# Performance work log

Measured on AMD Instinct MI355X. Metric: run time of the kernel, lower is better.

## Reference

```python
import jax, jax.numpy as jnp
import numpy as np

COMMITMENT = 0.25
THRESHOLD = 0.6
SNR_DB = 30.0  # eval_snr_db default-ish channel condition (fixed for determinism)
LN_EPS = 1e-5


def _layernorm(x, g, b):
    m = jnp.mean(x, axis=-1, keepdims=True)
    v = jnp.var(x, axis=-1, keepdims=True)
    return (x - m) * jax.lax.rsqrt(v + LN_EPS) * g + b


def _vq(x, codebook):
    # x: [T, D], codebook: [K, D]. Nearest-neighbor quantize + per-token VQ loss + STE.
    d = (x * x).sum(-1, keepdims=True) - 2.0 * (x @ codebook.T) + (codebook * codebook).sum(-1)  # [T, K]
    idx = jnp.argmin(d, axis=-1)
    q = codebook[idx]  # [T, D]
    loss = (COMMITMENT * jnp.mean((x - jax.lax.stop_gradient(q)) ** 2, axis=-1)
            + jnp.mean((jax.lax.stop_gradient(x) - q) ** 2, axis=-1))  # [T]
    q_ste = x + jax.lax.stop_gradient(q - x)
    return q_ste, loss


def setup_inputs() -> dict:
    key = jax.random.key(0)
    ks = jax.random.split(key, 8)
    B, N, De, Dq, Dd = 64, 196, 768, 512, 256
    return {
        'x_tokens': jax.random.normal(ks[0], (B, N, De), jnp.float32),
        'fim_logits': jax.random.normal(ks[1], (B, N, 1), jnp.float32),
        'W_proj': jax.random.normal(ks[2], (De, Dq), jnp.float32) * (1.0 / np.sqrt(De)),
        'b_proj': jnp.zeros((Dq,), jnp.float32),
        'ln_g': jnp.ones((Dq,), jnp.float32),
        'ln_b': jnp.zeros((Dq,), jnp.float32),
        'cb_high': jax.random.normal(ks[3], (4096, Dq), jnp.float32),
        'cb_low': jax.random.normal(ks[4], (256, Dq), jnp.float32),
        'W_dec': jax.random.normal(ks[5], (Dq, Dd), jnp.float32) * (1.0 / np.sqrt(Dq)),
        'b_dec': jnp.zeros((Dd,), jnp.float32),
        'h_ri': jax.random.normal(ks[6], (B, 2), jnp.float32),
        'noise': jax.random.normal(ks[7], (B, N, Dq), jnp.float32),
    }


def reference(x_tokens, fim_logits, W_proj, b_proj, ln_g, ln_b, cb_high, cb_low, W_dec, b_dec, h_ri, noise):
    B, N, _ = x_tokens.shape
    score = jax.nn.sigmoid(fim_logits[..., 0])          # [B, N]
    route_high = score > THRESHOLD                       # [B, N] bool

    x_proj = _layernorm(x_tokens @ W_proj + b_proj, ln_g, ln_b)  # [B, N, Dq]
    D = x_proj.shape[-1]
    xf = x_proj.reshape(-1, D)
    mf = route_high.reshape(-1)
    sf = score.reshape(-1)

    # Compute both experts densely, select with mask (same math as the masked
    # gather/scatter dispatch in the torch code, jit-friendly static shapes).
    q_high, loss_high = _vq(xf, cb_high)
    q_low, loss_low = _vq(xf, cb_low)
    final = jnp.where(mf[:, None], q_high, q_low).reshape(B, N, D)

    n_high = jnp.maximum(mf.sum(), 1)
    n_low = jnp.maximum((~mf).sum(), 1)
    vq_loss = (jnp.sum(jnp.where(mf, loss_high * sf, 0.0)) / n_high
               + jnp.sum(jnp.where(mf, 0.0, loss_low * (1.0 - sf))) / n_low) / 2.0

    # Rayleigh channel: per-sample fading magnitude h = |CN(0,1)|/sqrt(2), AWGN, equalize.
    n_var = 10.0 ** (-SNR_DB / 10.0)
    h = jnp.sqrt((h_ri ** 2).sum(-1)) / jnp.sqrt(2.0)    # [B]
    h = h[:, None, None]
    y = (h * final + jnp.sqrt(n_var) * noise) / h

    x_dec = y @ W_dec + b_dec                            # [B, N, 256]
    return x_dec, vq_loss
```

## Files before the change

### kernel.cpp

```cpp
#include <hip/hip_runtime.h>
#include <math.h>

#define T_TOK 12544
#define DE 768
#define DQ 512
#define DD 256
#define SEQ 196
#define NCH 4096
#define NCL 256
#define SPL_H 16
#define CODES_PER_BLK 256
#define MARGIN 2.0f
#define CAND_CAP 16

typedef __attribute__((ext_vector_type(8))) short s16x8;
typedef __attribute__((ext_vector_type(4))) float f32x4;

__device__ __forceinline__ float wave_reduce_sum(float v) {
    #pragma unroll
    for (int off = 32; off > 0; off >>= 1) v += __shfl_xor(v, off);
    return v;
}

__device__ __forceinline__ unsigned short f2bf(float f) {
    unsigned int u = __float_as_uint(f);
    u = (u + 0x7fffu + ((u >> 16) & 1u)) >> 16;
    return (unsigned short)u;
}
__device__ __forceinline__ float bf2f(unsigned short h) {
    return __uint_as_float(((unsigned int)h) << 16);
}

__device__ __forceinline__ void gload_lds16(const unsigned short* g, unsigned short* l) {
    __builtin_amdgcn_global_load_lds(
        (const __attribute__((address_space(1))) void*)g,
        (__attribute__((address_space(3))) void*)l,
        16, 0, 0);
}

__device__ __forceinline__ void sumsq_body(const float* __restrict__ cb,
                                           float* __restrict__ cs2,
                                           unsigned short* __restrict__ cbB,
                                           int blk, int NC) {
    int row = blk * 4 + (threadIdx.x >> 6);
    int lane = threadIdx.x & 63;
    if (row >= NC) return;
    const float4* p = (const float4*)(cb + (size_t)row * DQ);
    float4 a = p[lane];
    float4 b = p[lane + 64];
    if (cbB) {
        unsigned short* dst = cbB + (size_t)row * DQ;
        ushort4 ha, hb;
        ha.x = f2bf(a.x); ha.y = f2bf(a.y); ha.z = f2bf(a.z); ha.w = f2bf(a.w);
        hb.x = f2bf(b.x); hb.y = f2bf(b.y); hb.z = f2bf(b.z); hb.w = f2bf(b.w);
        *(ushort4*)(dst + lane * 4) = ha;
        *(ushort4*)(dst + 256 + lane * 4) = hb;
    }
    float s = a.x*a.x + a.y*a.y + a.z*a.z + a.w*a.w
            + b.x*b.x + b.y*b.y + b.z*b.z + b.w*b.w;
    s = wave_reduce_sum(s);
    if (lane == 0) cs2[row] = s;
}

__device__ __forceinline__ void split_body(const float* __restrict__ W, int K, int N,
                                           unsigned short* __restrict__ Thi,
                                           unsigned short* __restrict__ Tlo,
                                           int blk, int nb) {
    int total = K * N;
    for (int idx = blk * 256 + threadIdx.x; idx < total; idx += nb * 256) {
        int n = idx / K, k = idx - n * K;
        float v = W[(size_t)k * N + n];
        unsigned short h = f2bf(v);
        Thi[idx] = h;
        Tlo[idx] = f2bf(v - bf2f(h));
    }
}

__global__ __launch_bounds__(256) void prep_all(const float* __restrict__ cb_h,
                                                float* __restrict__ cs2h,
                                                unsigned short* __restrict__ cbhB,
                                                const float* __restrict__ cb_l,
                                                float* __restrict__ cs2l,
                                                unsigned short* __restrict__ cblB,
                                                const float* __restrict__ Wp,
                                                unsigned short* __restrict__ WThi,
                                                unsigned short* __restrict__ WTlo,
                                                const float* __restrict__ Wd,
                                                unsigned short* __restrict__ WdThi,
                                                unsigned short* __restrict__ WdTlo) {
    int blk = blockIdx.x;
    if (blk < 1024)       sumsq_body(cb_h, cs2h, cbhB, blk, NCH);
    else if (blk < 1088)  sumsq_body(cb_l, cs2l, cblB, blk - 1024, NCL);
    else if (blk < 1600)  split_body(Wp, DE, DQ, WThi, WTlo, blk - 1088, 512);
    else                  split_body(Wd, DQ, DD, WdThi, WdTlo, blk - 1600, 256);
}

template<int NC>
__global__ __launch_bounds__(256) void code_sumsq(const float* __restrict__ cb,
                                                  float* __restrict__ cs2) {
    sumsq_body(cb, cs2, nullptr, blockIdx.x, NC);
}

template<int KDIM, int NSTRIDE, int BN>
__global__ __launch_bounds__(256) void gemm_mfma3(const float* __restrict__ A,
                                                  const unsigned short* __restrict__ BThi,
                                                  const unsigned short* __restrict__ BTlo,
                                                  const float* __restrict__ bias,
                                                  float* __restrict__ out) {
    constexpr int CPW = BN / 64;
    __shared__ __align__(16) unsigned short Ahi[2][64 * 32];
    __shared__ __align__(16) unsigned short Alo[2][64 * 32];
    __shared__ __align__(16) unsigned short Bhi[2][BN * 32];
    __shared__ __align__(16) unsigned short Blo[2][BN * 32];
    const int m0 = blockIdx.x * 64, n0 = blockIdx.y * BN;
    const int tid = threadIdx.x, lane = tid & 63, w = tid >> 6;
    const int stok = tid >> 2, sslot = tid & 3;

    f32x4 acc[4][CPW] = {};
    float4 av0, av1;
    uint4 bh4[CPW], bl4[CPW];

    auto loadStep = [&](int k0) {
        const float* src = A + (size_t)(m0 + stok) * KDIM + k0 + sslot * 8;
        av0 = *(const float4*)src;
        av1 = *(const float4*)(src + 4);
        #pragma unroll
        for (int c = 0; c < CPW; c++) {
            size_t soff = (size_t)(n0 + c * 64 + stok) * KDIM + k0 + sslot * 8;
            bh4[c] = *(const uint4*)(BThi + soff);
            bl4[c] = *(const uint4*)(BTlo + soff);
        }
    };
    auto writeStep = [&](int buf) {
        float xv[8] = {av0.x, av0.y, av0.z, av0.w, av1.x, av1.y, av1.z, av1.w};
        unsigned int hw[4], lw[4];
        #pragma unroll
        for (int j = 0; j < 4; j++) {
            unsigned short h0 = f2bf(xv[2*j]),   h1 = f2bf(xv[2*j+1]);
            unsigned short l0 = f2bf(xv[2*j] - bf2f(h0));
            unsigned short l1 = f2bf(xv[2*j+1] - bf2f(h1));
            hw[j] = (unsigned)h0 | ((unsigned)h1 << 16);
            lw[j] = (unsigned)l0 | ((unsigned)l1 << 16);
        }
        int doffA = stok * 32 + (sslot ^ ((stok >> 1) & 3)) * 8;
        *(uint4*)&Ahi[buf][doffA] = make_uint4(hw[0], hw[1], hw[2], hw[3]);
        *(uint4*)&Alo[buf][doffA] = make_uint4(lw[0], lw[1], lw[2], lw[3]);
        #pragma unroll
        for (int c = 0; c < CPW; c++) {
            int col = c * 64 + stok;
            int doffB = col * 32 + (sslot ^ ((col >> 1) & 3)) * 8;
            *(uint4*)&Bhi[buf][doffB] = bh4[c];
            *(uint4*)&Blo[buf][doffB] = bl4[c];
        }
    };

    loadStep(0); writeStep(0); __syncthreads();
    const int NT = KDIM / 32;
    for (int t = 0; t < NT; t++) {
        const int cur = t & 1;
        if (t + 1 < NT) loadStep((t + 1) * 32);
        const int fr = lane & 15, fs = lane >> 4;
        s16x8 ah[4], al[4];
        #pragma unroll
        for (int tm = 0; tm < 4; tm++) {
            int tok = tm * 16 + fr;
            int off = tok * 32 + (fs ^ ((tok >> 1) & 3)) * 8;
            ah[tm] = *(const s16x8*)&Ahi[cur][off];
            al[tm] = *(const s16x8*)&Alo[cur][off];
        }
        #pragma unroll
        for (int n = 0; n < CPW; n++) {
            int col = w * (16 * CPW) + n * 16 + fr;
            int boff = col * 32 + (fs ^ ((col >> 1) & 3)) * 8;
            s16x8 bh = *(const s16x8*)&Bhi[cur][boff];
            s16x8 bl = *(const s16x8*)&Blo[cur][boff];
            #pragma unroll
            for (int tm = 0; tm < 4; tm++) {
                acc[tm][n] = __builtin_amdgcn_mfma_f32_16x16x32_bf16(ah[tm], bh, acc[tm][n], 0, 0, 0);
                acc[tm][n] = __builtin_amdgcn_mfma_f32_16x16x32_bf16(ah[tm], bl, acc[tm][n], 0, 0, 0);
                acc[tm][n] = __builtin_amdgcn_mfma_f32_16x16x32_bf16(al[tm], bh, acc[tm][n], 0, 0, 0);
            }
        }
        if (t + 1 < NT) writeStep(cur ^ 1);
        __syncthreads();
    }
    const int fr = lane & 15, fg = lane >> 4;
    #pragma unroll
    for (int n = 0; n < CPW; n++) {
        const int col = n0 + w * (16 * CPW) + n * 16 + fr;
        const float bb = bias[col];
        #pragma unroll
        for (int tm = 0; tm < 4; tm++) {
            #pragma unroll
            for (int r = 0; r < 4; r++) {
                int row = m0 + tm * 16 + fg * 4 + r;
                out[(size_t)row * NSTRIDE + col] = acc[tm][n][r] + bb;
            }
        }
    }
}

__global__ __launch_bounds__(256) void proj_gemm(const float* __restrict__ X,
                                                 const float* __restrict__ W,
                                                 const float* __restrict__ bias,
                                                 float* __restrict__ out) {
    __shared__ float As[32][66];
    __shared__ float Bs[32][64];
    const int m0 = blockIdx.x * 64, n0 = blockIdx.y * 64;
    const int tid = threadIdx.x;
    const int tx = tid & 15, ty = tid >> 4;
    float acc[4][4] = {};
    for (int k0 = 0; k0 < DE; k0 += 32) {
        {
            int e = tid;
            int r = e >> 3, c4 = e & 7;
            float4 v = *(const float4*)(X + (size_t)(m0 + r) * DE + k0 + c4 * 4);
            As[c4*4+0][r] = v.x; As[c4*4+1][r] = v.y; As[c4*4+2][r] = v.z; As[c4*4+3][r] = v.w;
            e = tid + 256;
            r = e >> 3; c4 = e & 7;
            v = *(const float4*)(X + (size_t)(m0 + r) * DE + k0 + c4 * 4);
            As[c4*4+0][r] = v.x; As[c4*4+1][r] = v.y; As[c4*4+2][r] = v.z; As[c4*4+3][r] = v.w;
        }
        {
            int e = tid;
            int kk = e >> 4, c4 = e & 15;
            *(float4*)&Bs[kk][c4*4] = *(const float4*)(W + (size_t)(k0 + kk) * DQ + n0 + c4 * 4);
            e = tid + 256;
            kk = e >> 4; c4 = e & 15;
            *(float4*)&Bs[kk][c4*4] = *(const float4*)(W + (size_t)(k0 + kk) * DQ + n0 + c4 * 4);
        }
        __syncthreads();
        #pragma unroll
        for (int k = 0; k < 32; k++) {
            float2 a01 = *(const float2*)&As[k][ty * 4];
            float2 a23 = *(const float2*)&As[k][ty * 4 + 2];
            float4 b = *(const float4*)&Bs[k][tx * 4];
            float av[4] = {a01.x, a01.y, a23.x, a23.y};
            float bv[4] = {b.x, b.y, b.z, b.w};
            #pragma unroll
            for (int i = 0; i < 4; i++)
                #pragma unroll
                for (int j = 0; j < 4; j++)
                    acc[i][j] += av[i] * bv[j];
        }
        __syncthreads();
    }
    float4 bv4 = *(const float4*)(bias + n0 + tx * 4);
    float bb[4] = {bv4.x, bv4.y, bv4.z, bv4.w};
    #pragma unroll
    for (int i = 0; i < 4; i++) {
        int row = m0 + ty * 4 + i;
        float4 o;
        o.x = acc[i][0] + bb[0];
        o.y = acc[i][1] + bb[1];
        o.z = acc[i][2] + bb[2];
        o.w = acc[i][3] + bb[3];
        *(float4*)(out + (size_t)row * DQ + n0 + tx * 4) = o;
    }
}

__global__ __launch_bounds__(256) void ln_route(float* __restrict__ xp,
                                                const float* __restrict__ g,
                                                const float* __restrict__ b,
                                                const float* __restrict__ logits,
                                                float* __restrict__ score,
                                                int* __restrict__ mask,
                                                unsigned short* __restrict__ xpB) {
    int row = blockIdx.x * 4 + (threadIdx.x >> 6);
    int lane = threadIdx.x & 63;
    float* p = xp + (size_t)row * DQ;
    float4 v0 = *(float4*)(p + lane * 4);
    float4 v1 = *(float4*)(p + 256 + lane * 4);
    float s  = v0.x + v0.y + v0.z + v0.w + v1.x + v1.y + v1.z + v1.w;
    float ss = v0.x*v0.x + v0.y*v0.y + v0.z*v0.z + v0.w*v0.w
             + v1.x*v1.x + v1.y*v1.y + v1.z*v1.z + v1.w*v1.w;
    s = wave_reduce_sum(s);
    ss = wave_reduce_sum(ss);
    float m = s * (1.f / DQ);
    float var = ss * (1.f / DQ) - m * m;
    float scale = rsqrtf(var + 1e-5f);
    float4 g0 = *(const float4*)(g + lane * 4);
    float4 g1 = *(const float4*)(g + 256 + lane * 4);
    float4 b0 = *(const float4*)(b + lane * 4);
    float4 b1 = *(const float4*)(b + 256 + lane * 4);
    float4 o0, o1;
    o0.x = (v0.x - m) * scale * g0.x + b0.x;
    o0.y = (v0.y - m) * scale * g0.y + b0.y;
    o0.z = (v0.z - m) * scale * g0.z + b0.z;
    o0.w = (v0.w - m) * scale * g0.w + b0.w;
    o1.x = (v1.x - m) * scale * g1.x + b1.x;
    o1.y = (v1.y - m) * scale * g1.y + b1.y;
    o1.z = (v1.z - m) * scale * g1.z + b1.z;
    o1.w = (v1.w - m) * scale * g1.w + b1.w;
    *(float4*)(p + lane * 4) = o0;
    *(float4*)(p + 256 + lane * 4) = o1;
    if (xpB) {
        unsigned short* dst = xpB + (size_t)row * DQ;
        ushort4 h0, h1;
        h0.x = f2bf(o0.x); h0.y = f2bf(o0.y); h0.z = f2bf(o0.z); h0.w = f2bf(o0.w);
        h1.x = f2bf(o1.x); h1.y = f2bf(o1.y); h1.z = f2bf(o1.z); h1.w = f2bf(o1.w);
        *(ushort4*)(dst + lane * 4) = h0;
        *(ushort4*)(dst + 256 + lane * 4) = h1;
    }
    if (lane == 0) {
        float lg = logits[row];
        float sc = 1.f / (1.f + expf(-lg));
        score[row] = sc;
        mask[row] = sc > 0.6f ? 1 : 0;
    }
}

__global__ __launch_bounds__(1024) void scan_compact(const int* __restrict__ mask,
                                                     int* __restrict__ hlist,
                                                     int* __restrict__ llist,
                                                     int* __restrict__ counts) {
    __shared__ int wsum[16];
    __shared__ int base_h, base_l;
    int tid = threadIdx.x, lane = tid & 63, wid = tid >> 6;
    if (tid == 0) { base_h = 0; base_l = 0; }
    __syncthreads();
    for (int t0 = 0; t0 < T_TOK; t0 += 1024) {
        int t = t0 + tid;
        int valid = t < T_TOK;
        int m = valid ? mask[t] : 0;
        unsigned long long bal = __ballot(m);
        int pre = __popcll(bal & ((1ull << lane) - 1ull));
        if (lane == 0) wsum[wid] = __popcll(bal);
        __syncthreads();
        int woff = 0;
        for (int w = 0; w < wid; w++) woff += wsum[w];
        int btot = 0;
        for (int w = 0; w < 16; w++) btot += wsum[w];
        int vcnt = T_TOK - t0; if (vcnt > 1024) vcnt = 1024;
        int bh = base_h, bl = base_l;
        if (valid) {
            if (m) hlist[bh + woff + pre] = t;
            else   llist[bl + (tid - (woff + pre))] = t;
        }
        __syncthreads();
        if (tid == 0) { base_h = bh + btot; base_l = bl + (vcnt - btot); }
        __syncthreads();
    }
    if (tid == 0) { counts[0] = base_h; counts[1] = base_l; }
}

__global__ __launch_bounds__(256) void vq_mfma_all(const unsigned short* __restrict__ xpB,
                                                   const unsigned short* __restrict__ cbhB,
                                                   const float* __restrict__ cs2h,
                                                   const int* __restrict__ hlist,
                                                   const unsigned short* __restrict__ cblB,
                                                   const float* __restrict__ cs2l,
                                                   const int* __restrict__ llist,
                                                   const int* __restrict__ counts,
                                                   float* __restrict__ smaxH,
                                                   int* __restrict__ scntH,
                                                   uint2* __restrict__ candH,
                                                   float* __restrict__ smaxL,
                                                   int* __restrict__ scntL,
                                                   uint2* __restrict__ candL) {
    const int by = blockIdx.y;
    const unsigned short* cbB; const float* cs2; const int* list;
    float* smax; int* scnt; uint2* cand;
    int count, slice, SPLIT;
    if (by < SPL_H) {
        cbB = cbhB; cs2 = cs2h; list = hlist; count = counts[0];
        slice = by; SPLIT = SPL_H; smax = smaxH; scnt = scntH; cand = candH;
    } else {
        cbB = cblB; cs2 = cs2l; list = llist; count = counts[1];
        slice = 0; SPLIT = 1; smax = smaxL; scnt = scntL; cand = candL;
    }
    const int base = blockIdx.x * 64;
    if (base >= count) return;
    const int cbase = slice * CODES_PER_BLK;

    __shared__ __align__(16) unsigned short Abuf[2 * 64 * 32];
    __shared__ __align__(16) unsigned short Bbuf[2 * 256 * 32];
    __shared__ float wmaxs[4][64];
    __shared__ float tokmax[64];
    __shared__ int ccnt[64];
    __shared__ uint2 cland[64][CAND_CAP];
    __shared__ int rows_s[64];

    const int tid = threadIdx.x;
    const int lane = tid & 63;
    const int w = tid >> 6;
    const int stok = tid >> 2, sslot = tid & 3;

    if (tid < 64) {
        int tl = base + tid;
        rows_s[tid] = list[tl < count ? tl : (count - 1)];
        ccnt[tid] = 0;
    }
    __syncthreads();

    const int swz = sslot ^ ((stok >> 1) & 3);
    const unsigned short* gA  = xpB + (size_t)rows_s[stok] * DQ + swz * 8;
    const unsigned short* gB0 = cbB + (size_t)(cbase + 0 * 64 + stok) * DQ + swz * 8;
    const unsigned short* gB1 = cbB + (size_t)(cbase + 1 * 64 + stok) * DQ + swz * 8;
    const unsigned short* gB2 = cbB + (size_t)(cbase + 2 * 64 + stok) * DQ + swz * 8;
    const unsigned short* gB3 = cbB + (size_t)(cbase + 3 * 64 + stok) * DQ + swz * 8;
    unsigned short* dA = Abuf + w * 512;
    unsigned short* dB = Bbuf + w * 512;

    auto stage = [&](int buf, int k0) {
        gload_lds16(gA  + k0, dA + buf * (64 * 32));
        gload_lds16(gB0 + k0, dB + buf * (256 * 32) + 0 * 2048);
        gload_lds16(gB1 + k0, dB + buf * (256 * 32) + 1 * 2048);
        gload_lds16(gB2 + k0, dB + buf * (256 * 32) + 2 * 2048);
        gload_lds16(gB3 + k0, dB + buf * (256 * 32) + 3 * 2048);
    };

    f32x4 acc[4][4] = {};

    stage(0, 0);
    __syncthreads();
    const int NT = DQ / 32;
    for (int t = 0; t < NT; t++) {
        const int cur = t & 1;
        if (t + 1 < NT) stage(cur ^ 1, (t + 1) * 32);
        const int fr = lane & 15, fs = lane >> 4;
        s16x8 af[4], bf[4];
        #pragma unroll
        for (int tm = 0; tm < 4; tm++) {
            int tok = tm * 16 + fr;
            af[tm] = *(const s16x8*)&Abuf[cur * (64 * 32) + tok * 32 + (fs ^ ((tok >> 1) & 3)) * 8];
        }
        #pragma unroll
        for (int tn = 0; tn < 4; tn++) {
            int cl = w * 64 + tn * 16 + fr;
            bf[tn] = *(const s16x8*)&Bbuf[cur * (256 * 32) + cl * 32 + (fs ^ ((cl >> 1) & 3)) * 8];
        }
        #pragma unroll
        for (int tm = 0; tm < 4; tm++)
            #pragma unroll
            for (int tn = 0; tn < 4; tn++)
                acc[tm][tn] = __builtin_amdgcn_mfma_f32_16x16x32_bf16(af[tm], bf[tn], acc[tm][tn], 0, 0, 0);
        __syncthreads();
    }

    const int fr = lane & 15, fg = lane >> 4;
    float c2[4];
    #pragma unroll
    for (int tn = 0; tn < 4; tn++) c2[tn] = 0.5f * cs2[cbase + w * 64 + tn * 16 + fr];

    #pragma unroll
    for (int tm = 0; tm < 4; tm++) {
        #pragma unroll
        for (int r = 0; r < 4; r++) {
            float m4 = -3.0e38f;
            #pragma unroll
            for (int tn = 0; tn < 4; tn++) {
                float s = acc[tm][tn][r] - c2[tn];
                m4 = fmaxf(m4, s);
            }
            #pragma unroll
            for (int off = 1; off < 16; off <<= 1)
                m4 = fmaxf(m4, __shfl_xor(m4, off));
            if (fr == 0) wmaxs[w][tm * 16 + fg * 4 + r] = m4;
        }
    }
    __syncthreads();
    if (tid < 64)
        tokmax[tid] = fmaxf(fmaxf(wmaxs[0][tid], wmaxs[1][tid]),
                            fmaxf(wmaxs[2][tid], wmaxs[3][tid]));
    __syncthreads();

    #pragma unroll
    for (int tm = 0; tm < 4; tm++) {
        #pragma unroll
        for (int r = 0; r < 4; r++) {
            int token = tm * 16 + fg * 4 + r;
            float thr = tokmax[token] - MARGIN;
            #pragma unroll
            for (int tn = 0; tn < 4; tn++) {
                float s = acc[tm][tn][r] - c2[tn];
                if (s > thr) {
                    int pos = atomicAdd(&ccnt[token], 1);
                    if (pos < CAND_CAP) {
                        uint2 cd;
                        cd.x = __float_as_uint(s);
                        cd.y = (unsigned)(cbase + w * 64 + tn * 16 + fr);
                        cland[token][pos] = cd;
                    }
                }
            }
        }
    }
    __syncthreads();

    if (tid < 64) {
        int tl = base + tid;
        if (tl < count) {
            smax[(size_t)tl * SPLIT + slice] = tokmax[tid];
            scnt[(size_t)tl * SPLIT + slice] = min(ccnt[tid], CAND_CAP);
        }
    }
    for (int i = tid; i < 64 * CAND_CAP; i += 256) {
        int token = i >> 4, j = i & (CAND_CAP - 1);
        int tl = base + token;
        if (tl < count && j < min(ccnt[token], CAND_CAP))
            cand[((size_t)tl * SPLIT + slice) * CAND_CAP + j] = cland[token][j];
    }
}

__global__ __launch_bounds__(256) void vq_rescore_all(float* __restrict__ xp,
                                                      const float* __restrict__ cb_h,
                                                      const float* __restrict__ smaxH,
                                                      const int* __restrict__ scntH,
                                                      const uint2* __restrict__ candH,
                                                      const int* __restrict__ hlist,
                                                      const float* __restrict__ cb_l,
                                                      const float* __restrict__ smaxL,
                                                      const int* __restrict__ scntL,
                                                      const uint2* __restrict__ candL,
                                                      const int* __restrict__ llist,
                                                      const int* __restrict__ counts,
                                                      int* __restrict__ out_idx,
                                                      const float* __restrict__ noise,
                                                      const float* __restrict__ h_ri,
                                                      const float* __restrict__ score,
                                                      float* __restrict__ lh,
                                                      float* __restrict__ ll) {
    const int HB = T_TOK / 4;
    int bx = blockIdx.x;
    const float* cb; const float* smax; const int* scnt; const uint2* cand; const int* list;
    int count, SPLIT, cidx;
    if (bx < HB) {
        cb = cb_h; smax = smaxH; scnt = scntH; cand = candH; list = hlist;
        count = counts[0]; SPLIT = SPL_H; cidx = 0;
    } else {
        bx -= HB;
        cb = cb_l; smax = smaxL; scnt = scntL; cand = candL; list = llist;
        count = counts[1]; SPLIT = 1; cidx = 1;
    }
    const int wid = threadIdx.x >> 6;
    const int lane = threadIdx.x & 63;
    const int tl = bx * 4 + wid;
    if (tl >= count) return;

    float gm = -3.0e38f;
    if (lane < SPLIT) gm = smax[(size_t)tl * SPLIT + lane];
    #pragma unroll
    for (int off = 1; off < 64; off <<= 1)
        gm = fmaxf(gm, __shfl_xor(gm, off));
    const float thr = gm - MARGIN;

    const int t = list[tl];
    float xv[8];
    #pragma unroll
    for (int kk = 0; kk < 8; kk++) xv[kk] = xp[(size_t)t * DQ + lane * 8 + kk];

    double bs = -1.0e300;
    int bi = 0x7fffffff;
    for (int s = 0; s < SPLIT; s++) {
        int cn = scnt[(size_t)tl * SPLIT + s];
        for (int j = 0; j < cn; j++) {
            uint2 cd = cand[((size_t)tl * SPLIT + s) * CAND_CAP + j];
            float av = __uint_as_float(cd.x);
            if (av >= thr) {
                int code = (int)cd.y;
                const float* crow = cb + (size_t)code * DQ;
                double dot = 0.0, nrm = 0.0;
                #pragma unroll
                for (int kk = 0; kk < 8; kk++) {
                    double cv = (double)crow[lane * 8 + kk];
                    dot += (double)xv[kk] * cv;
                    nrm += cv * cv;
                }
                #pragma unroll
                for (int off = 1; off < 64; off <<= 1) {
                    dot += __shfl_xor(dot, off);
                    nrm += __shfl_xor(nrm, off);
                }
                double sc = dot - 0.5 * nrm;
                if (sc > bs || (sc == bs && code < bi)) { bs = sc; bi = code; }
            }
        }
    }
    const float* qrow = cb + (size_t)bi * DQ;
    float4 q0 = *(const float4*)(qrow + lane * 8);
    float4 q1 = *(const float4*)(qrow + lane * 8 + 4);
    const float* nz = noise + (size_t)t * DQ;
    float4 n0 = *(const float4*)(nz + lane * 8);
    float4 n1 = *(const float4*)(nz + lane * 8 + 4);
    float ds = 0.f, dx;
    dx = xv[0] - q0.x; ds += dx * dx;
    dx = xv[1] - q0.y; ds += dx * dx;
    dx = xv[2] - q0.z; ds += dx * dx;
    dx = xv[3] - q0.w; ds += dx * dx;
    dx = xv[4] - q1.x; ds += dx * dx;
    dx = xv[5] - q1.y; ds += dx * dx;
    dx = xv[6] - q1.z; ds += dx * dx;
    dx = xv[7] - q1.w; ds += dx * dx;
    ds = wave_reduce_sum(ds);
    int bbt = t / SEQ;
    float hh0 = h_ri[bbt * 2], hh1 = h_ri[bbt * 2 + 1];
    float hh = sqrtf((hh0 * hh0 + hh1 * hh1) * 0.5f);
    float cc = sqrtf(1e-3f) / hh;
    float4 y0, y1;
    y0.x = q0.x + cc * n0.x; y0.y = q0.y + cc * n0.y;
    y0.z = q0.z + cc * n0.z; y0.w = q0.w + cc * n0.w;
    y1.x = q1.x + cc * n1.x; y1.y = q1.y + cc * n1.y;
    y1.z = q1.z + cc * n1.z; y1.w = q1.w + cc * n1.w;
    *(float4*)(xp + (size_t)t * DQ + lane * 8) = y0;
    *(float4*)(xp + (size_t)t * DQ + lane * 8 + 4) = y1;
    if (lane == 0) {
        out_idx[t] = bi;
        float loss = 1.25f * ds * (1.f / DQ);
        float sc = score[t];
        if (cidx == 0) { lh[t] = loss * sc;  ll[t] = 0.f; }
        else           { lh[t] = 0.f;        ll[t] = loss * (1.f - sc); }
    }
}

template<int NC, int SPLIT>
__global__ __launch_bounds__(256) void vq_partial(const float* __restrict__ xp,
                                                  const float* __restrict__ cb,
                                                  const float* __restrict__ cs2,
                                                  const int* __restrict__ list,
                                                  const int* __restrict__ counts,
                                                  int cidx,
                                                  float* __restrict__ part_s,
                                                  int* __restrict__ part_i) {
    const int count = counts[cidx];
    const int base = blockIdx.x * 64;
    if (base >= count) return;
    const int CODES = NC / SPLIT;
    const int cbase = blockIdx.y * CODES;
    __shared__ float As[32][68];
    __shared__ float Cs[32][68];
    __shared__ int rows_s[64];
    const int tid = threadIdx.x;
    if (tid < 64) {
        int tl = base + tid;
        rows_s[tid] = list[tl < count ? tl : (count - 1)];
    }
    __syncthreads();
    const int tx = tid & 15, ty = tid >> 4;
    float best_s[4];
    int best_i[4];
    #pragma unroll
    for (int i = 0; i < 4; i++) { best_s[i] = -3.0e38f; best_i[i] = 0; }
    for (int c0 = cbase; c0 < cbase + CODES; c0 += 64) {
        float acc[4][4] = {};
        for (int k0 = 0; k0 < DQ; k0 += 32) {
            {
                int e = tid;
                int r = e >> 3, c4 = e & 7;
                float4 v = *(const float4*)(xp + (size_t)rows_s[r] * DQ + k0 + c4 * 4);
                As[c4*4+0][r] = v.x; As[c4*4+1][r] = v.y; As[c4*4+2][r] = v.z; As[c4*4+3][r] = v.w;
                e = tid + 256; r = e >> 3; c4 = e & 7;
                v = *(const float4*)(xp + (size_t)rows_s[r] * DQ + k0 + c4 * 4);
                As[c4*4+0][r] = v.x; As[c4*4+1][r] = v.y; As[c4*4+2][r] = v.z; As[c4*4+3][r] = v.w;
            }
            {
                int e = tid;
                int r = e >> 3, c4 = e & 7;
                float4 v = *(const float4*)(cb + (size_t)(c0 + r) * DQ + k0 + c4 * 4);
                Cs[c4*4+0][r] = v.x; Cs[c4*4+1][r] = v.y; Cs[c4*4+2][r] = v.z; Cs[c4*4+3][r] = v.w;
                e = tid + 256; r = e >> 3; c4 = e & 7;
                v = *(const float4*)(cb + (size_t)(c0 + r) * DQ + k0 + c4 * 4);
                Cs[c4*4+0][r] = v.x; Cs[c4*4+1][r] = v.y; Cs[c4*4+2][r] = v.z; Cs[c4*4+3][r] = v.w;
            }
            __syncthreads();
            #pragma unroll
            for (int k = 0; k < 32; k++) {
                float4 a = *(const float4*)&As[k][ty * 4];
                float4 b = *(const float4*)&Cs[k][tx * 4];
                float av[4] = {a.x, a.y, a.z, a.w};
                float bv[4] = {b.x, b.y, b.z, b.w};
                #pragma unroll
                for (int i = 0; i < 4; i++)
                    #pragma unroll
                    for (int j = 0; j < 4; j++)
                        acc[i][j] += av[i] * bv[j];
            }
            __syncthreads();
        }
        float4 c2v = *(const float4*)(cs2 + c0 + tx * 4);
        float c2[4] = {c2v.x, c2v.y, c2v.z, c2v.w};
        #pragma unroll
        for (int i = 0; i < 4; i++) {
            float s = acc[i][0] - 0.5f * c2[0];
            int bi = c0 + tx * 4;
            #pragma unroll
            for (int j = 1; j < 4; j++) {
                float sj = acc[i][j] - 0.5f * c2[j];
                if (sj > s) { s = sj; bi = c0 + tx * 4 + j; }
            }
            #pragma unroll
            for (int off = 1; off < 16; off <<= 1) {
                float os = __shfl_xor(s, off);
                int oi = __shfl_xor(bi, off);
                if (os > s || (os == s && oi < bi)) { s = os; bi = oi; }
            }
            if (s > best_s[i] || (s == best_s[i] && bi < best_i[i])) {
                best_s[i] = s; best_i[i] = bi;
            }
        }
    }
    if (tx == 0) {
        #pragma unroll
        for (int i = 0; i < 4; i++) {
            int tl = base + ty * 4 + i;
            if (tl < count) {
                part_s[(size_t)tl * SPLIT + blockIdx.y] = best_s[i];
                part_i[(size_t)tl * SPLIT + blockIdx.y] = best_i[i];
            }
        }
    }
}

template<int SPLIT>
__global__ __launch_bounds__(256) void vq_reduce(const float* __restrict__ part_s,
                                                 const int* __restrict__ part_i,
                                                 const int* __restrict__ list,
                                                 const int* __restrict__ counts,
                                                 int cidx,
                                                 int* __restrict__ out_idx) {
    int tl = blockIdx.x * 256 + threadIdx.x;
    if (tl >= counts[cidx]) return;
    float bs = part_s[(size_t)tl * SPLIT];
    int bi = part_i[(size_t)tl * SPLIT];
    #pragma unroll
    for (int s = 1; s < SPLIT; s++) {
        float v = part_s[(size_t)tl * SPLIT + s];
        int vi = part_i[(size_t)tl * SPLIT + s];
        if (v > bs || (v == bs && vi < bi)) { bs = v; bi = vi; }
    }
    out_idx[list[tl]] = bi;
}

__global__ __launch_bounds__(256) void gather_loss_y(float* __restrict__ xp,
                                                     const float* __restrict__ cb_h,
                                                     const float* __restrict__ cb_l,
                                                     const int* __restrict__ idx,
                                                     const float* __restrict__ score,
                                                     const int* __restrict__ mask,
                                                     const float* __restrict__ noise,
                                                     const float* __restrict__ h_ri,
                                                     float* __restrict__ lh,
                                                     float* __restrict__ ll) {
    int t = blockIdx.x * 4 + (threadIdx.x >> 6);
    int lane = threadIdx.x & 63;
    int m = mask[t];
    float sc = score[t];
    const float* q = (m ? cb_h : cb_l) + (size_t)idx[t] * DQ;
    float* x = xp + (size_t)t * DQ;
    const float* nz = noise + (size_t)t * DQ;
    int bb = t / SEQ;
    float h0 = h_ri[bb * 2], h1 = h_ri[bb * 2 + 1];
    float h = sqrtf((h0 * h0 + h1 * h1) * 0.5f);
    float c = sqrtf(1e-3f) / h;
    float4 xv0 = *(float4*)(x + lane * 4);
    float4 xv1 = *(float4*)(x + 256 + lane * 4);
    float4 qv0 = *(const float4*)(q + lane * 4);
    float4 qv1 = *(const float4*)(q + 256 + lane * 4);
    float4 nv0 = *(const float4*)(nz + lane * 4);
    float4 nv1 = *(const float4*)(nz + 256 + lane * 4);
    float dx, ds = 0.f;
    dx = xv0.x - qv0.x; ds += dx * dx;
    dx = xv0.y - qv0.y; ds += dx * dx;
    dx = xv0.z - qv0.z; ds += dx * dx;
    dx = xv0.w - qv0.w; ds += dx * dx;
    dx = xv1.x - qv1.x; ds += dx * dx;
    dx = xv1.y - qv1.y; ds += dx * dx;
    dx = xv1.z - qv1.z; ds += dx * dx;
    dx = xv1.w - qv1.w; ds += dx * dx;
    ds = wave_reduce_sum(ds);
    float4 y0, y1;
    y0.x = qv0.x + c * nv0.x; y0.y = qv0.y + c * nv0.y;
    y0.z = qv0.z + c * nv0.z; y0.w = qv0.w + c * nv0.w;
    y1.x = qv1.x + c * nv1.x; y1.y = qv1.y + c * nv1.y;
    y1.z = qv1.z + c * nv1.z; y1.w = qv1.w + c * nv1.w;
    *(float4*)(x + lane * 4) = y0;
    *(float4*)(x + 256 + lane * 4) = y1;
    if (lane == 0) {
        float loss = 1.25f * ds * (1.f / DQ);
        lh[t] = m ? loss * sc : 0.f;
        ll[t] = m ? 0.f : loss * (1.f - sc);
    }
}

__global__ __launch_bounds__(256) void loss_reduce(const float* __restrict__ lh,
                                                   const float* __restrict__ ll,
                                                   const int* __restrict__ counts,
                                                   float* __restrict__ out) {
    __shared__ float sh[256], sl[256];
    int tid = threadIdx.x;
    float ah = 0.f, al = 0.f;
    for (int t = tid; t < T_TOK; t += 256) { ah += lh[t]; al += ll[t]; }
    sh[tid] = ah; sl[tid] = al;
    __syncthreads();
    for (int o = 128; o > 0; o >>= 1) {
        if (tid < o) { sh[tid] += sh[tid + o]; sl[tid] += sl[tid + o]; }
        __syncthreads();
    }
    if (tid == 0) {
        int nh = counts[0];
        int nl = T_TOK - nh;
        nh = nh > 1 ? nh : 1;
        nl = nl > 1 ? nl : 1;
        out[(size_t)T_TOK * DD] = 0.5f * (sh[0] / (float)nh + sl[0] / (float)nl);
    }
}

__global__ __launch_bounds__(256) void dec_gemm(const float* __restrict__ Y,
                                                const float* __restrict__ W,
                                                const float* __restrict__ bias,
                                                float* __restrict__ out) {
    __shared__ float As[32][66];
    __shared__ float Bs[32][64];
    const int m0 = blockIdx.x * 64, n0 = blockIdx.y * 64;
    const int tid = threadIdx.x;
    const int tx = tid & 15, ty = tid >> 4;
    float acc[4][4] = {};
    for (int k0 = 0; k0 < DQ; k0 += 32) {
        {
            int e = tid;
            int r = e >> 3, c4 = e & 7;
            float4 v = *(const float4*)(Y + (size_t)(m0 + r) * DQ + k0 + c4 * 4);
            As[c4*4+0][r] = v.x; As[c4*4+1][r] = v.y; As[c4*4+2][r] = v.z; As[c4*4+3][r] = v.w;
            e = tid + 256; r = e >> 3; c4 = e & 7;
            v = *(const float4*)(Y + (size_t)(m0 + r) * DQ + k0 + c4 * 4);
            As[c4*4+0][r] = v.x; As[c4*4+1][r] = v.y; As[c4*4+2][r] = v.z; As[c4*4+3][r] = v.w;
        }
        {
            int e = tid;
            int kk = e >> 4, c4 = e & 15;
            *(float4*)&Bs[kk][c4*4] = *(const float4*)(W + (size_t)(k0 + kk) * DD + n0 + c4 * 4);
            e = tid + 256; kk = e >> 4; c4 = e & 15;
            *(float4*)&Bs[kk][c4*4] = *(const float4*)(W + (size_t)(k0 + kk) * DD + n0 + c4 * 4);
        }
        __syncthreads();
        #pragma unroll
        for (int k = 0; k < 32; k++) {
            float2 a01 = *(const float2*)&As[k][ty * 4];
            float2 a23 = *(const float2*)&As[k][ty * 4 + 2];
            float4 b = *(const float4*)&Bs[k][tx * 4];
            float av[4] = {a01.x, a01.y, a23.x, a23.y};
            float bv[4] = {b.x, b.y, b.z, b.w};
            #pragma unroll
            for (int i = 0; i < 4; i++)
                #pragma unroll
                for (int j = 0; j < 4; j++)
                    acc[i][j] += av[i] * bv[j];
        }
        __syncthreads();
    }
    float4 bv4 = *(const float4*)(bias + n0 + tx * 4);
    float bbv[4] = {bv4.x, bv4.y, bv4.z, bv4.w};
    #pragma unroll
    for (int i = 0; i < 4; i++) {
        int row = m0 + ty * 4 + i;
        float4 o;
        o.x = acc[i][0] + bbv[0];
        o.y = acc[i][1] + bbv[1];
        o.z = acc[i][2] + bbv[2];
        o.w = acc[i][3] + bbv[3];
        *(float4*)(out + (size_t)row * DD + n0 + tx * 4) = o;
    }
}

extern "C" void kernel_launch(void* const* d_in, const int* in_sizes, int n_in,
                              void* d_out, int out_size, void* d_ws, size_t ws_size,
                              hipStream_t stream) {
    const float* x_tokens = (const float*)d_in[0];
    const float* fim      = (const float*)d_in[1];
    const float* W_proj   = (const float*)d_in[2];
    const float* b_proj   = (const float*)d_in[3];
    const float* ln_g     = (const float*)d_in[4];
    const float* ln_b     = (const float*)d_in[5];
    const float* cb_high  = (const float*)d_in[6];
    const float* cb_low   = (const float*)d_in[7];
    const float* W_dec    = (const float*)d_in[8];
    const float* b_dec    = (const float*)d_in[9];
    const float* h_ri     = (const float*)d_in[10];
    const float* noise    = (const float*)d_in[11];
    float* out = (float*)d_out;

    char* ws = (char*)d_ws;
    size_t off = 0;
    float* xp = (float*)(ws + off);     off += (size_t)T_TOK * DQ * 4;
    int*   idxb = (int*)(ws + off);     off += (size_t)T_TOK * 4;
    float* score = (float*)(ws + off);  off += (size_t)T_TOK * 4;
    int*   mask = (int*)(ws + off);     off += (size_t)T_TOK * 4;
    float* lh = (float*)(ws + off);     off += (size_t)T_TOK * 4;
    float* ll = (float*)(ws + off);     off += (size_t)T_TOK * 4;
    int*   hlist = (int*)(ws + off);    off += (size_t)T_TOK * 4;
    int*   llist = (int*)(ws + off);    off += (size_t)T_TOK * 4;
    int*   counts = (int*)(ws + off);   off += 64;
    float* cs2h = (float*)(ws + off);   off += (size_t)NCH * 4;
    float* cs2l = (float*)(ws + off);   off += (size_t)NCL * 4;
    size_t off_common = off;

    unsigned short* xpB  = (unsigned short*)(ws + off); off += (size_t)T_TOK * DQ * 2;
    unsigned short* cbhB = (unsigned short*)(ws + off); off += (size_t)NCH * DQ * 2;
    unsigned short* cblB = (unsigned short*)(ws + off); off += (size_t)NCL * DQ * 2;
    float* smaxH = (float*)(ws + off);  off += (size_t)T_TOK * SPL_H * 4;
    int*   scntH = (int*)(ws + off);    off += (size_t)T_TOK * SPL_H * 4;
    uint2* candH = (uint2*)(ws + off);  off += (size_t)T_TOK * SPL_H * CAND_CAP * 8;
    float* smaxL = (float*)(ws + off);  off += (size_t)T_TOK * 4;
    int*   scntL = (int*)(ws + off);    off += (size_t)T_TOK * 4;
    uint2* candL = (uint2*)(ws + off);  off += (size_t)T_TOK * CAND_CAP * 8;
    unsigned short* WThi  = (unsigned short*)(ws + off); off += (size_t)DQ * DE * 2;
    unsigned short* WTlo  = (unsigned short*)(ws + off); off += (size_t)DQ * DE * 2;
    unsigned short* WdThi = (unsigned short*)(ws + off); off += (size_t)DD * DQ * 2;
    unsigned short* WdTlo = (unsigned short*)(ws + off); off += (size_t)DD * DQ * 2;
    size_t need_new = off;
    const bool use_mfma = ws_size >= need_new;

    if (use_mfma) {
        prep_all<<<1856, 256, 0, stream>>>(cb_high, cs2h, cbhB, cb_low, cs2l, cblB,
                                           W_proj, WThi, WTlo, W_dec, WdThi, WdTlo);
        gemm_mfma3<DE, DQ, 64><<<dim3(T_TOK / 64, DQ / 64), 256, 0, stream>>>(
            x_tokens, WThi, WTlo, b_proj, xp);
        ln_route<<<T_TOK / 4, 256, 0, stream>>>(xp, ln_g, ln_b, fim, score, mask, xpB);
        scan_compact<<<1, 1024, 0, stream>>>(mask, hlist, llist, counts);
        vq_mfma_all<<<dim3(T_TOK / 64, SPL_H + 1), 256, 0, stream>>>(
            xpB, cbhB, cs2h, hlist, cblB, cs2l, llist, counts,
            smaxH, scntH, candH, smaxL, scntL, candL);
        vq_rescore_all<<<2 * (T_TOK / 4), 256, 0, stream>>>(
            xp, cb_high, smaxH, scntH, candH, hlist,
            cb_low, smaxL, scntL, candL, llist,
            counts, idxb, noise, h_ri, score, lh, ll);
        loss_reduce<<<1, 256, 0, stream>>>(lh, ll, counts, out);
        gemm_mfma3<DQ, DD, 64><<<dim3(T_TOK / 64, DD / 64), 256, 0, stream>>>(
            xp, WdThi, WdTlo, b_dec, out);
    } else {
        code_sumsq<NCH><<<NCH / 4, 256, 0, stream>>>(cb_high, cs2h);
        code_sumsq<NCL><<<NCL / 4, 256, 0, stream>>>(cb_low, cs2l);
        proj_gemm<<<dim3(T_TOK / 64, DQ / 64), 256, 0, stream>>>(x_tokens, W_proj, b_proj, xp);
        ln_route<<<T_TOK / 4, 256, 0, stream>>>(xp, ln_g, ln_b, fim, score, mask, nullptr);
        scan_compact<<<1, 1024, 0, stream>>>(mask, hlist, llist, counts);
        float* part_s = (float*)(ws + off_common);
        int*   part_i = (int*)(ws + off_common + (size_t)T_TOK * 16 * 4);
        vq_partial<NCH, 16><<<dim3(T_TOK / 64, 16), 256, 0, stream>>>(
            xp, cb_high, cs2h, hlist, counts, 0, part_s, part_i);
        vq_reduce<16><<<(T_TOK + 255) / 256, 256, 0, stream>>>(part_s, part_i, hlist, counts, 0, idxb);
        vq_partial<NCL, 4><<<dim3(T_TOK / 64, 4), 256, 0, stream>>>(
            xp, cb_low, cs2l, llist, counts, 1, part_s, part_i);
        vq_reduce<4><<<(T_TOK + 255) / 256, 256, 0, stream>>>(part_s, part_i, llist, counts, 1, idxb);
        gather_loss_y<<<T_TOK / 4, 256, 0, stream>>>(xp, cb_high, cb_low, idxb, score, mask,
                                                     noise, h_ri, lh, ll);
        loss_reduce<<<1, 256, 0, stream>>>(lh, ll, counts, out);
        dec_gemm<<<dim3(T_TOK / 64, DD / 64), 256, 0, stream>>>(xp, W_dec, b_dec, out);
    }
}
```

Measured before the change: 217.5 us.

## Shrink VQ MFMA block to 32 tokens and drop LDS double buffering

The VQ distance kernel now processes 32 tokens per block instead of 64, doubling the grid along tokens. It also drops the double-buffered LDS staging for a single buffer loaded at each k-step, followed by a barrier. The aim is to cut LDS use and accumulator registers so more blocks are resident and the partially empty grid is better balanced. In exchange, codebook tiles are re-read for twice as many token blocks, and global loads no longer overlap MFMA work within a block.

```diff
diff --git a/kernel.cpp b/kernel.cpp
--- a/kernel.cpp
+++ b/kernel.cpp
@@ -12,6 +12,7 @@
 #define CODES_PER_BLK 256
 #define MARGIN 2.0f
 #define CAND_CAP 16
+#define VQTOK 32
 
 typedef __attribute__((ext_vector_type(8))) short s16x8;
 typedef __attribute__((ext_vector_type(4))) float f32x4;
@@ -369,24 +370,24 @@
         cbB = cblB; cs2 = cs2l; list = llist; count = counts[1];
         slice = 0; SPLIT = 1; smax = smaxL; scnt = scntL; cand = candL;
     }
-    const int base = blockIdx.x * 64;
+    const int base = blockIdx.x * VQTOK;
     if (base >= count) return;
     const int cbase = slice * CODES_PER_BLK;
 
-    __shared__ __align__(16) unsigned short Abuf[2 * 64 * 32];
-    __shared__ __align__(16) unsigned short Bbuf[2 * 256 * 32];
-    __shared__ float wmaxs[4][64];
-    __shared__ float tokmax[64];
-    __shared__ int ccnt[64];
-    __shared__ uint2 cland[64][CAND_CAP];
-    __shared__ int rows_s[64];
+    __shared__ __align__(16) unsigned short Abuf[VQTOK * 32];
+    __shared__ __align__(16) unsigned short Bbuf[256 * 32];
+    __shared__ float wmaxs[4][VQTOK];
+    __shared__ float tokmax[VQTOK];
+    __shared__ int ccnt[VQTOK];
+    __shared__ uint2 cland[VQTOK][CAND_CAP];
+    __shared__ int rows_s[VQTOK];
 
     const int tid = threadIdx.x;
     const int lane = tid & 63;
     const int w = tid >> 6;
     const int stok = tid >> 2, sslot = tid & 3;
 
-    if (tid < 64) {
+    if (tid < VQTOK) {
         int tl = base + tid;
         rows_s[tid] = list[tl < count ? tl : (count - 1)];
         ccnt[tid] = 0;
@@ -394,7 +395,7 @@
     __syncthreads();
 
     const int swz = sslot ^ ((stok >> 1) & 3);
-    const unsigned short* gA  = xpB + (size_t)rows_s[stok] * DQ + swz * 8;
+    const unsigned short* gA  = xpB + (size_t)rows_s[stok & (VQTOK - 1)] * DQ + swz * 8;
     const unsigned short* gB0 = cbB + (size_t)(cbase + 0 * 64 + stok) * DQ + swz * 8;
     const unsigned short* gB1 = cbB + (size_t)(cbase + 1 * 64 + stok) * DQ + swz * 8;
     const unsigned short* gB2 = cbB + (size_t)(cbase + 2 * 64 + stok) * DQ + swz * 8;
@@ -402,36 +403,31 @@
     unsigned short* dA = Abuf + w * 512;
     unsigned short* dB = Bbuf + w * 512;
 
-    auto stage = [&](int buf, int k0) {
-        gload_lds16(gA  + k0, dA + buf * (64 * 32));
-        gload_lds16(gB0 + k0, dB + buf * (256 * 32) + 0 * 2048);
-        gload_lds16(gB1 + k0, dB + buf * (256 * 32) + 1 * 2048);
-        gload_lds16(gB2 + k0, dB + buf * (256 * 32) + 2 * 2048);
-        gload_lds16(gB3 + k0, dB + buf * (256 * 32) + 3 * 2048);
-    };
-
-    f32x4 acc[4][4] = {};
-
-    stage(0, 0);
-    __syncthreads();
+    f32x4 acc[2][4] = {};
+
     const int NT = DQ / 32;
     for (int t = 0; t < NT; t++) {
-        const int cur = t & 1;
-        if (t + 1 < NT) stage(cur ^ 1, (t + 1) * 32);
+        const int k0 = t * 32;
+        if (w < 2) gload_lds16(gA + k0, dA);
+        gload_lds16(gB0 + k0, dB + 0 * 2048);
+        gload_lds16(gB1 + k0, dB + 1 * 2048);
+        gload_lds16(gB2 + k0, dB + 2 * 2048);
+        gload_lds16(gB3 + k0, dB + 3 * 2048);
+        __syncthreads();
         const int fr = lane & 15, fs = lane >> 4;
-        s16x8 af[4], bf[4];
-        #pragma unroll
-        for (int tm = 0; tm < 4; tm++) {
+        s16x8 af[2], bf[4];
+        #pragma unroll
+        for (int tm = 0; tm < 2; tm++) {
             int tok = tm * 16 + fr;
-            af[tm] = *(const s16x8*)&Abuf[cur * (64 * 32) + tok * 32 + (fs ^ ((tok >> 1) & 3)) * 8];
+            af[tm] = *(const s16x8*)&Abuf[tok * 32 + (fs ^ ((tok >> 1) & 3)) * 8];
         }
         #pragma unroll
         for (int tn = 0; tn < 4; tn++) {
             int cl = w * 64 + tn * 16 + fr;
-            bf[tn] = *(const s16x8*)&Bbuf[cur * (256 * 32) + cl * 32 + (fs ^ ((cl >> 1) & 3)) * 8];
-        }
-        #pragma unroll
-        for (int tm = 0; tm < 4; tm++)
+            bf[tn] = *(const s16x8*)&Bbuf[cl * 32 + (fs ^ ((cl >> 1) & 3)) * 8];
+        }
+        #pragma unroll
+        for (int tm = 0; tm < 2; tm++)
             #pragma unroll
             for (int tn = 0; tn < 4; tn++)
                 acc[tm][tn] = __builtin_amdgcn_mfma_f32_16x16x32_bf16(af[tm], bf[tn], acc[tm][tn], 0, 0, 0);
@@ -444,7 +440,7 @@
     for (int tn = 0; tn < 4; tn++) c2[tn] = 0.5f * cs2[cbase + w * 64 + tn * 16 + fr];
 
     #pragma unroll
-    for (int tm = 0; tm < 4; tm++) {
+    for (int tm = 0; tm < 2; tm++) {
         #pragma unroll
         for (int r = 0; r < 4; r++) {
             float m4 = -3.0e38f;
@@ -460,13 +456,13 @@
         }
     }
     __syncthreads();
-    if (tid < 64)
+    if (tid < VQTOK)
         tokmax[tid] = fmaxf(fmaxf(wmaxs[0][tid], wmaxs[1][tid]),
                             fmaxf(wmaxs[2][tid], wmaxs[3][tid]));
     __syncthreads();
 
     #pragma unroll
-    for (int tm = 0; tm < 4; tm++) {
+    for (int tm = 0; tm < 2; tm++) {
         #pragma unroll
         for (int r = 0; r < 4; r++) {
             int token = tm * 16 + fg * 4 + r;
@@ -488,14 +484,14 @@
     }
     __syncthreads();
 
-    if (tid < 64) {
+    if (tid < VQTOK) {
         int tl = base + tid;
         if (tl < count) {
             smax[(size_t)tl * SPLIT + slice] = tokmax[tid];
             scnt[(size_t)tl * SPLIT + slice] = min(ccnt[tid], CAND_CAP);
         }
     }
-    for (int i = tid; i < 64 * CAND_CAP; i += 256) {
+    for (int i = tid; i < VQTOK * CAND_CAP; i += 256) {
         int token = i >> 4, j = i & (CAND_CAP - 1);
         int tl = base + token;
         if (tl < count && j < min(ccnt[token], CAND_CAP))
@@ -917,7 +913,7 @@
             x_tokens, WThi, WTlo, b_proj, xp);
         ln_route<<<T_TOK / 4, 256, 0, stream>>>(xp, ln_g, ln_b, fim, score, mask, xpB);
         scan_compact<<<1, 1024, 0, stream>>>(mask, hlist, llist, counts);
-        vq_mfma_all<<<dim3(T_TOK / 64, SPL_H + 1), 256, 0, stream>>>(
+        vq_mfma_all<<<dim3(T_TOK / VQTOK, SPL_H + 1), 256, 0, stream>>>(
             xpB, cbhB, cs2h, hlist, cblB, cs2l, llist, counts,
             smaxH, scntH, candH, smaxL, scntL, candL);
         vq_rescore_all<<<2 * (T_TOK / 4), 256, 0, stream>>>(
```

Result: no change. 219.6 us (+1.0%).
